# Kernel tuning notes

Hardware: AMD Instinct MI355X
Metric: run time of the kernel (lower is better)

Reference implementation:

```python
import jax, jax.numpy as jnp
import numpy as np

B, T, I = 512, 512, 32
H = 64
NUM_TICKERS = 8


def setup_inputs() -> dict:
    key = jax.random.key(0)
    ks = jax.random.split(key, 8)
    s = 1.0 / np.sqrt(H)  # PyTorch LSTM init scale
    x = jax.random.normal(ks[0], (B, T, I), dtype=jnp.float32)
    w_ih = jax.random.uniform(ks[1], (4 * H, I), minval=-s, maxval=s, dtype=jnp.float32)
    w_hh = jax.random.uniform(ks[2], (4 * H, H), minval=-s, maxval=s, dtype=jnp.float32)
    b_ih = jax.random.uniform(ks[3], (4 * H,), minval=-s, maxval=s, dtype=jnp.float32)
    b_hh = jax.random.uniform(ks[4], (4 * H,), minval=-s, maxval=s, dtype=jnp.float32)
    sf = 1.0 / np.sqrt(H)
    w_fc = jax.random.uniform(ks[5], (NUM_TICKERS, H), minval=-sf, maxval=sf, dtype=jnp.float32)
    b_fc = jax.random.uniform(ks[6], (NUM_TICKERS,), minval=-sf, maxval=sf, dtype=jnp.float32)
    return {"x": x, "w_ih": w_ih, "w_hh": w_hh, "b_ih": b_ih, "b_hh": b_hh,
            "w_fc": w_fc, "b_fc": b_fc}


def _lstm_last_h(x, w_ih, w_hh, b_ih, b_hh):
    # Precompute input projection for all timesteps: (T, B, 4H)
    xproj = jnp.einsum('bti,gi->tbg', x, w_ih) + (b_ih + b_hh)
    h0 = jnp.zeros((x.shape[0], H), x.dtype)
    c0 = jnp.zeros((x.shape[0], H), x.dtype)

    def step(carry, xt):
        h, c = carry
        gates = xt + h @ w_hh.T                      # (B, 4H)
        i, f, g, o = jnp.split(gates, 4, axis=-1)    # PyTorch gate order i,f,g,o
        i = jax.nn.sigmoid(i)
        f = jax.nn.sigmoid(f)
        g = jnp.tanh(g)
        o = jax.nn.sigmoid(o)
        c = f * c + i * g
        h = o * jnp.tanh(c)
        return (h, c), None

    (h_last, _), _ = jax.lax.scan(step, (h0, c0), xproj)
    return h_last  # == out[:, -1, :]


def reference(x, w_ih, w_hh, b_ih, b_hh, w_fc, b_fc):
    h_last = _lstm_last_h(x, w_ih, w_hh, b_ih, b_hh)
    return h_last @ w_fc.T + b_fc  # (B, num_tickers)
```

## Files before the change

kernel.cpp:

```cpp
#include <hip/hip_runtime.h>

#define TT 512
#define ID 32
#define HD 64
#define NTK 8
#define RPB 4
#define ZPAD 80

typedef __attribute__((ext_vector_type(8))) _Float16 half8;
typedef __attribute__((ext_vector_type(2))) __fp16 fp16x2;
typedef __attribute__((ext_vector_type(4))) float f32x4;

#define L2E 1.44269504089f

__device__ __forceinline__ f32x4 MF(half8 a, half8 b, f32x4 c) {
    return __builtin_amdgcn_mfma_f32_16x16x32_f16(a, b, c, 0, 0, 0);
}

__device__ __forceinline__ half8 cvt8(float4 a, float4 b) {
    union { fp16x2 h2[4]; half8 h8; } u;
    u.h2[0] = __builtin_amdgcn_cvt_pkrtz(a.x, a.y);
    u.h2[1] = __builtin_amdgcn_cvt_pkrtz(a.z, a.w);
    u.h2[2] = __builtin_amdgcn_cvt_pkrtz(b.x, b.y);
    u.h2[3] = __builtin_amdgcn_cvt_pkrtz(b.z, b.w);
    return u.h8;
}

__global__ __launch_bounds__(256, 1) void lstm8(
    const float* __restrict__ x,
    const float* __restrict__ w_ih,
    const float* __restrict__ w_hh,
    const float* __restrict__ b_ih,
    const float* __restrict__ b_hh,
    const float* __restrict__ w_fc,
    const float* __restrict__ b_fc,
    float* __restrict__ out)
{
    const int tid = threadIdx.x;
    const int wv  = tid >> 6;
    const int l   = tid & 63;
    const int l15 = l & 15;
    const int lq  = l >> 4;
    const int abr = l15 >> 2;
    const int sst = l15 & 3;
    const int r0  = blockIdx.x * RPB;

    __shared__ __align__(16) _Float16 zbuf[2][RPB][ZPAD];

    half8 Bh0[4], Bh1[4], Bx[4];
    f32x4 biasC[4];
    #pragma unroll
    for (int nt = 0; nt < 4; ++nt) {
        const int n = nt * 64 + wv * 16 + l15;
        const float bias = b_ih[n] + b_hh[n];
        biasC[nt] = (f32x4){bias, bias, bias, bias};
        const float* ph = w_hh + n * HD + lq * 8;
        float4 p0 = ((const float4*)ph)[0], p1 = ((const float4*)ph)[1];
        Bh0[nt] = (half8){(_Float16)p0.x, (_Float16)p0.y, (_Float16)p0.z, (_Float16)p0.w,
                          (_Float16)p1.x, (_Float16)p1.y, (_Float16)p1.z, (_Float16)p1.w};
        p0 = ((const float4*)(ph + 32))[0]; p1 = ((const float4*)(ph + 32))[1];
        Bh1[nt] = (half8){(_Float16)p0.x, (_Float16)p0.y, (_Float16)p0.z, (_Float16)p0.w,
                          (_Float16)p1.x, (_Float16)p1.y, (_Float16)p1.z, (_Float16)p1.w};
        const float* px = w_ih + n * ID + lq * 8;
        p0 = ((const float4*)px)[0]; p1 = ((const float4*)px)[1];
        Bx[nt]  = (half8){(_Float16)p0.x, (_Float16)p0.y, (_Float16)p0.z, (_Float16)p0.w,
                          (_Float16)p1.x, (_Float16)p1.y, (_Float16)p1.z, (_Float16)p1.w};
    }

    zbuf[0][tid >> 6][tid & 63] = (_Float16)0.0f;

    const float* xbase = x + ((size_t)(r0 + abr) * TT + sst) * ID + lq * 8;

    float4 xaf0, xaf1, xbf0, xbf1;
    xaf0 = ((const float4*)xbase)[0]; xaf1 = ((const float4*)xbase)[1];
    half8 xc = cvt8(xaf0, xaf1);
    f32x4 xpA_O = MF(xc, Bx[3], biasC[3]);
    f32x4 xpA_F = MF(xc, Bx[1], biasC[1]);
    f32x4 xpA_I = MF(xc, Bx[0], biasC[0]);
    f32x4 xpA_G = MF(xc, Bx[2], biasC[2]);
    xbf0 = ((const float4*)(xbase + 4 * ID))[0];
    xbf1 = ((const float4*)(xbase + 4 * ID))[1];
    half8 xn0h = cvt8(xbf0, xbf1);
    half8 xn1h;
    f32x4 xpB_O, xpB_F, xpB_I, xpB_G;
    float c_ = 0.0f;
    __syncthreads();

#define STEP(S, RB, WB, XPO, XPF, XPI, XPG, XBUILD)                                 \
    {                                                                               \
        half8 z0 = *(const half8*)&zbuf[RB][abr][lq * 8];                           \
        half8 z1 = *(const half8*)&zbuf[RB][abr][32 + lq * 8];                      \
        XBUILD;                                                                     \
        f32x4 aO = MF(z0, Bh0[3], XPO);                                             \
        f32x4 aF = MF(z0, Bh0[1], XPF);                                             \
        f32x4 aI = MF(z0, Bh0[0], XPI);                                             \
        f32x4 aG = MF(z0, Bh0[2], XPG);                                             \
        aO = MF(z1, Bh1[3], aO);                                                    \
        aF = MF(z1, Bh1[1], aF);                                                    \
        aI = MF(z1, Bh1[0], aI);                                                    \
        aG = MF(z1, Bh1[2], aG);                                                    \
        const float eo = __builtin_amdgcn_exp2f(-L2E * aO[S]);                      \
        const float ef = __builtin_amdgcn_exp2f(-L2E * aF[S]);                      \
        const float ei = __builtin_amdgcn_exp2f(-L2E * aI[S]);                      \
        const float to = 1.0f + eo;                                                 \
        const float rf = __builtin_amdgcn_rcpf(1.0f + ef);                          \
        const float ti = 1.0f + ei;                                                 \
        const float eg = __builtin_amdgcn_exp2f(fminf(2.0f * L2E * aG[S], 60.0f));  \
        const float rig = __builtin_amdgcn_rcpf(fmaf(eg, ti, ti));                  \
        c_ = fmaf(c_, rf, fmaf(eg, rig, -rig));                                     \
        const float ec = __builtin_amdgcn_exp2f(fminf(2.0f * L2E * c_, 60.0f));     \
        const float rh = __builtin_amdgcn_rcpf(fmaf(ec, to, to));                   \
        const float hh = fmaf(ec, rh, -rh);                                         \
        zbuf[WB][lq][wv * 16 + l15] = (_Float16)hh;                                 \
    }

    for (int t = 0; t < TT; t += 8) {
        const int tA = (t + 8  < TT) ? t + 8  : t;
        const int tB = (t + 12 < TT) ? t + 12 : t;
        STEP(0, 0, 1, xpA_O, xpA_F, xpA_I, xpA_G,
             { const float* s_ = xbase + (size_t)tA * ID;
               xaf0 = ((const float4*)s_)[0]; xaf1 = ((const float4*)s_)[1];
               xpB_O = MF(xn0h, Bx[3], biasC[3]); });
        __syncthreads();
        STEP(1, 1, 0, xpA_O, xpA_F, xpA_I, xpA_G,
             { xpB_F = MF(xn0h, Bx[1], biasC[1]); });
        __syncthreads();
        STEP(2, 0, 1, xpA_O, xpA_F, xpA_I, xpA_G,
             { xpB_I = MF(xn0h, Bx[0], biasC[0]); });
        __syncthreads();
        STEP(3, 1, 0, xpA_O, xpA_F, xpA_I, xpA_G,
             { xpB_G = MF(xn0h, Bx[2], biasC[2]);
               xn1h = cvt8(xaf0, xaf1); });
        __syncthreads();
        STEP(0, 0, 1, xpB_O, xpB_F, xpB_I, xpB_G,
             { const float* s_ = xbase + (size_t)tB * ID;
               xbf0 = ((const float4*)s_)[0]; xbf1 = ((const float4*)s_)[1];
               xpA_O = MF(xn1h, Bx[3], biasC[3]); });
        __syncthreads();
        STEP(1, 1, 0, xpB_O, xpB_F, xpB_I, xpB_G,
             { xpA_F = MF(xn1h, Bx[1], biasC[1]); });
        __syncthreads();
        STEP(2, 0, 1, xpB_O, xpB_F, xpB_I, xpB_G,
             { xpA_I = MF(xn1h, Bx[0], biasC[0]); });
        __syncthreads();
        STEP(3, 1, 0, xpB_O, xpB_F, xpB_I, xpB_G,
             { xpA_G = MF(xn1h, Bx[2], biasC[2]);
               xn0h = cvt8(xbf0, xbf1); });
        __syncthreads();
    }
#undef STEP

    if (tid < RPB * NTK) {
        const int rr = tid >> 3;
        const int tk = tid & 7;
        float a = b_fc[tk];
        const float* wf = w_fc + tk * HD;
        #pragma unroll
        for (int j = 0; j < HD; ++j)
            a = fmaf((float)zbuf[0][rr][j], wf[j], a);
        out[(r0 + rr) * NTK + tk] = a;
    }
}

extern "C" void kernel_launch(void* const* d_in, const int* in_sizes, int n_in,
                              void* d_out, int out_size, void* d_ws, size_t ws_size,
                              hipStream_t stream) {
    const float* x    = (const float*)d_in[0];
    const float* w_ih = (const float*)d_in[1];
    const float* w_hh = (const float*)d_in[2];
    const float* b_ih = (const float*)d_in[3];
    const float* b_hh = (const float*)d_in[4];
    const float* w_fc = (const float*)d_in[5];
    const float* b_fc = (const float*)d_in[6];
    float* out = (float*)d_out;

    const int nx = in_sizes[0];
    const int B  = nx / (TT * ID);

    lstm8<<<dim3(B / RPB), dim3(256), 0, stream>>>(x, w_ih, w_hh, b_ih, b_hh,
                                                   w_fc, b_fc, out);
}
```

Measured before the change: 143.1 us.

## Stage whole per-block x sequence in LDS as fp16 before recurrence

```diff
diff --git a/kernel.cpp b/kernel.cpp
--- a/kernel.cpp
+++ b/kernel.cpp
@@ -6,6 +6,10 @@
 #define NTK 8
 #define RPB 4
 #define ZPAD 80
+#define XPITCH_H 16448
+#define XBYTES   (RPB * XPITCH_H * 2)
+#define ZBYTES   (2 * RPB * ZPAD * 2)
+#define SHBYTES  (XBYTES + ZBYTES)
 
 typedef __attribute__((ext_vector_type(8))) _Float16 half8;
 typedef __attribute__((ext_vector_type(2))) __fp16 fp16x2;
@@ -26,7 +30,7 @@
     return u.h8;
 }
 
-__global__ __launch_bounds__(256, 1) void lstm8(
+__global__ __launch_bounds__(256, 1) void lstm9(
     const float* __restrict__ x,
     const float* __restrict__ w_ih,
     const float* __restrict__ w_hh,
@@ -36,6 +40,10 @@
     const float* __restrict__ b_fc,
     float* __restrict__ out)
 {
+    extern __shared__ __align__(16) char smem[];
+    _Float16* xlds = (_Float16*)smem;
+    _Float16 (*zbuf)[RPB][ZPAD] = (_Float16 (*)[RPB][ZPAD])(smem + XBYTES);
+
     const int tid = threadIdx.x;
     const int wv  = tid >> 6;
     const int l   = tid & 63;
@@ -44,8 +52,6 @@
     const int abr = l15 >> 2;
     const int sst = l15 & 3;
     const int r0  = blockIdx.x * RPB;
-
-    __shared__ __align__(16) _Float16 zbuf[2][RPB][ZPAD];
 
     half8 Bh0[4], Bh1[4], Bx[4];
     f32x4 biasC[4];
@@ -67,24 +73,35 @@
                           (_Float16)p1.x, (_Float16)p1.y, (_Float16)p1.z, (_Float16)p1.w};
     }
 
+    #pragma unroll
+    for (int r = 0; r < RPB; ++r) {
+        const float4* src = (const float4*)(x + ((size_t)(r0 + r) * TT) * ID);
+        _Float16* dst = xlds + r * XPITCH_H;
+        #pragma unroll
+        for (int k = 0; k < 8; ++k) {
+            const int c = tid + k * 256;
+            float4 a = src[2 * c];
+            float4 b = src[2 * c + 1];
+            *(half8*)(dst + c * 8) = cvt8(a, b);
+        }
+    }
     zbuf[0][tid >> 6][tid & 63] = (_Float16)0.0f;
+    __syncthreads();
 
-    const float* xbase = x + ((size_t)(r0 + abr) * TT + sst) * ID + lq * 8;
+    const _Float16* xlane = xlds + abr * XPITCH_H + (sst * 4 + lq) * 8;
+    auto ldsx = [&](int t) -> half8 {
+        return *(const half8*)(xlane + t * (4 * 8));
+    };
 
-    float4 xaf0, xaf1, xbf0, xbf1;
-    xaf0 = ((const float4*)xbase)[0]; xaf1 = ((const float4*)xbase)[1];
-    half8 xc = cvt8(xaf0, xaf1);
+    half8 xc = ldsx(0);
     f32x4 xpA_O = MF(xc, Bx[3], biasC[3]);
     f32x4 xpA_F = MF(xc, Bx[1], biasC[1]);
     f32x4 xpA_I = MF(xc, Bx[0], biasC[0]);
     f32x4 xpA_G = MF(xc, Bx[2], biasC[2]);
-    xbf0 = ((const float4*)(xbase + 4 * ID))[0];
-    xbf1 = ((const float4*)(xbase + 4 * ID))[1];
-    half8 xn0h = cvt8(xbf0, xbf1);
-    half8 xn1h;
+    half8 xn0 = ldsx(4);
+    half8 xn1;
     f32x4 xpB_O, xpB_F, xpB_I, xpB_G;
     float c_ = 0.0f;
-    __syncthreads();
 
 #define STEP(S, RB, WB, XPO, XPF, XPI, XPG, XBUILD)                                 \
     {                                                                               \
@@ -118,34 +135,28 @@
         const int tA = (t + 8  < TT) ? t + 8  : t;
         const int tB = (t + 12 < TT) ? t + 12 : t;
         STEP(0, 0, 1, xpA_O, xpA_F, xpA_I, xpA_G,
-             { const float* s_ = xbase + (size_t)tA * ID;
-               xaf0 = ((const float4*)s_)[0]; xaf1 = ((const float4*)s_)[1];
-               xpB_O = MF(xn0h, Bx[3], biasC[3]); });
+             { xn1 = ldsx(tA); xpB_O = MF(xn0, Bx[3], biasC[3]); });
         __syncthreads();
         STEP(1, 1, 0, xpA_O, xpA_F, xpA_I, xpA_G,
-             { xpB_F = MF(xn0h, Bx[1], biasC[1]); });
+             { xpB_F = MF(xn0, Bx[1], biasC[1]); });
         __syncthreads();
         STEP(2, 0, 1, xpA_O, xpA_F, xpA_I, xpA_G,
-             { xpB_I = MF(xn0h, Bx[0], biasC[0]); });
+             { xpB_I = MF(xn0, Bx[0], biasC[0]); });
         __syncthreads();
         STEP(3, 1, 0, xpA_O, xpA_F, xpA_I, xpA_G,
-             { xpB_G = MF(xn0h, Bx[2], biasC[2]);
-               xn1h = cvt8(xaf0, xaf1); });
+             { xpB_G = MF(xn0, Bx[2], biasC[2]); });
         __syncthreads();
         STEP(0, 0, 1, xpB_O, xpB_F, xpB_I, xpB_G,
-             { const float* s_ = xbase + (size_t)tB * ID;
-               xbf0 = ((const float4*)s_)[0]; xbf1 = ((const float4*)s_)[1];
-               xpA_O = MF(xn1h, Bx[3], biasC[3]); });
+             { xn0 = ldsx(tB); xpA_O = MF(xn1, Bx[3], biasC[3]); });
         __syncthreads();
         STEP(1, 1, 0, xpB_O, xpB_F, xpB_I, xpB_G,
-             { xpA_F = MF(xn1h, Bx[1], biasC[1]); });
+             { xpA_F = MF(xn1, Bx[1], biasC[1]); });
         __syncthreads();
         STEP(2, 0, 1, xpB_O, xpB_F, xpB_I, xpB_G,
-             { xpA_I = MF(xn1h, Bx[0], biasC[0]); });
+             { xpA_I = MF(xn1, Bx[0], biasC[0]); });
         __syncthreads();
         STEP(3, 1, 0, xpB_O, xpB_F, xpB_I, xpB_G,
-             { xpA_G = MF(xn1h, Bx[2], biasC[2]);
-               xn0h = cvt8(xbf0, xbf1); });
+             { xpA_G = MF(xn1, Bx[2], biasC[2]); });
         __syncthreads();
     }
 #undef STEP
@@ -177,6 +188,11 @@
     const int nx = in_sizes[0];
     const int B  = nx / (TT * ID);
 
-    lstm8<<<dim3(B / RPB), dim3(256), 0, stream>>>(x, w_ih, w_hh, b_ih, b_hh,
-                                                   w_fc, b_fc, out);
+    static int attr_done = 0;
+    (void)hipFuncSetAttribute((const void*)lstm9,
+                              hipFuncAttributeMaxDynamicSharedMemorySize, SHBYTES);
+    (void)attr_done;
+
+    lstm9<<<dim3(B / RPB), dim3(256), SHBYTES, stream>>>(x, w_ih, w_hh, b_ih, b_hh,
+                                                         w_fc, b_fc, out);
 }
```

Measured after the change: 119.0 us. -16.8%, faster.
